# Performance work log

Measured on AMD Instinct MI355X. Metric: run time of the kernel, lower is better.

Reference implementation:

```python
import jax, jax.numpy as jnp
import numpy as np

NCE_T = 0.07   # opt.nce_T
EPS = 1e-8     # torch CosineSimilarity eps
DIAG_FILL = -10.0

N, D = 8192, 256

def setup_inputs() -> dict:
    key = jax.random.key(0)
    kq, kk = jax.random.split(key)
    feat_q = jax.random.normal(kq, (N, D), dtype=jnp.float32)
    feat_k = jax.random.normal(kk, (N, D), dtype=jnp.float32)
    return {"feat_q": feat_q, "feat_k": feat_k}

def reference(feat_q, feat_k):
    # feat_k is detached in the original
    feat_k = jax.lax.stop_gradient(feat_k)
    nq = jnp.linalg.norm(feat_q, axis=-1)            # [N]
    nk = jnp.linalg.norm(feat_k, axis=-1)            # [N]
    # positive cosine similarity (paired rows)
    l_pos = jnp.sum(feat_q * feat_k, axis=-1) / jnp.maximum(nq * nk, EPS)  # [N]
    # full N x N cosine similarity via GEMM (torch does a broadcasted version)
    sim = (feat_q @ feat_k.T) / jnp.maximum(nq[:, None] * nk[None, :], EPS)  # [N,N]
    # mask self-similarities with -10.0 BEFORE dividing by temperature
    diag = jnp.eye(sim.shape[0], dtype=bool)
    l_neg = jnp.where(diag, DIAG_FILL, sim)
    out = jnp.concatenate([l_pos[:, None], l_neg], axis=1) / NCE_T  # [N, N+1]
    # cross-entropy vs target class 0, reduction='none'
    loss = jax.scipy.special.logsumexp(out, axis=1) - out[:, 0]     # [N]
    return loss
```

## Files before the change

kernel.cpp:

```cpp
#include <hip/hip_runtime.h>
#include <stdint.h>
#include <math.h>

#define NROWS 8192
#define DDIM  256
#define BM    128
#define BN    128
#define GJ    8
#define COLS_PER_GROUP (NROWS / GJ)

constexpr float INV_T  = 1.0f / 0.07f;
constexpr float LOG2E  = 1.44269504f;
constexpr float K1     = INV_T * LOG2E;

typedef __bf16 bf16x8 __attribute__((ext_vector_type(8)));
typedef float  f32x4  __attribute__((ext_vector_type(4)));

__device__ __forceinline__ void async_copy16(const uint16_t* g, uint16_t* l) {
    __builtin_amdgcn_global_load_lds(
        (const __attribute__((address_space(1))) uint32_t*)g,
        (__attribute__((address_space(3))) uint32_t*)l, 16, 0, 0);
}

__device__ inline uint16_t f2bf(float f) {
    uint32_t u = __float_as_uint(f);
    u += 0x7fffu + ((u >> 16) & 1u);
    return (uint16_t)(u >> 16);
}

__global__ __launch_bounds__(256) void norm_convert_kernel(
    const float* __restrict__ fq, const float* __restrict__ fk,
    uint16_t* __restrict__ qb, uint16_t* __restrict__ kb)
{
    const int wave = threadIdx.x >> 6;
    const int lane = threadIdx.x & 63;
    const int row  = blockIdx.x * 4 + wave;

    const float* src; uint16_t* dstb;
    if (row < NROWS) {
        src = fq + (size_t)row * DDIM; dstb = qb + (size_t)row * DDIM;
    } else {
        int r = row - NROWS;
        src = fk + (size_t)r * DDIM; dstb = kb + (size_t)r * DDIM;
    }

    float4 v = ((const float4*)src)[lane];
    float ss = v.x*v.x + v.y*v.y + v.z*v.z + v.w*v.w;
    #pragma unroll
    for (int m = 1; m < 64; m <<= 1) ss += __shfl_xor(ss, m, 64);
    float r = rsqrtf(ss);

    ushort4 o;
    o.x = f2bf(v.x * r); o.y = f2bf(v.y * r); o.z = f2bf(v.z * r); o.w = f2bf(v.w * r);
    ((ushort4*)dstb)[lane] = o;
}

__global__ __launch_bounds__(512, 2) void nce_main_kernel(
    const uint16_t* __restrict__ qb, const uint16_t* __restrict__ kb,
    float* __restrict__ lpT, float* __restrict__ gpl)
{
    __shared__ __align__(16) uint16_t lds_k[4 * BN * 32];

    const int tid    = threadIdx.x;
    const int wave   = tid >> 6;
    const int lane   = tid & 63;
    const int quad   = lane >> 4;
    const int lanelo = lane & 15;
    const int wr     = wave >> 1;
    const int wc     = wave & 1;
    const int rowBase      = blockIdx.x * BM;
    const int colGroupBase = blockIdx.y * COLS_PER_GROUP;

    bf16x8 aq[2][8];
    #pragma unroll
    for (int mt = 0; mt < 2; ++mt) {
        const uint16_t* qrow =
            qb + (size_t)(rowBase + wr * 32 + mt * 16 + lanelo) * DDIM + quad * 8;
        #pragma unroll
        for (int kk = 0; kk < 8; ++kk)
            aq[mt][kk] = *(const bf16x8*)(qrow + kk * 32);
    }

    const int kS   = wave * 64 + lane;
    const int krow = kS >> 2;
    const int kch  = (lane & 3) ^ ((krow >> 2) & 3);
    const uint16_t* kbase = kb + (size_t)(colGroupBase + krow) * DDIM + kch * 8;

    #pragma unroll
    for (int p = 0; p < 3; ++p)
        async_copy16(kbase + (p << 5), lds_k + (p << 12) + (wave << 9));

    int bvoff[4];
    #pragma unroll
    for (int nt = 0; nt < 4; ++nt) {
        int rk = wc * 64 + nt * 16 + lanelo;
        bvoff[nt] = rk * 32 + (quad ^ (lanelo >> 2)) * 8;
    }

    float l_run[8];
    #pragma unroll
    for (int i = 0; i < 8; ++i) l_run[i] = 0.f;

    for (int jt = 0; jt < 8; ++jt) {
        const int colT = colGroupBase + jt * BN;

        f32x4 acc[2][4];
        #pragma unroll
        for (int mt = 0; mt < 2; ++mt)
            #pragma unroll
            for (int nt = 0; nt < 4; ++nt)
                acc[mt][nt] = (f32x4){0.f, 0.f, 0.f, 0.f};

        #pragma unroll
        for (int kk = 0; kk < 8; ++kk) {
            const int p = (jt << 3) + kk;

            asm volatile("s_waitcnt vmcnt(2)" ::: "memory");
            asm volatile("s_barrier" ::: "memory");

            {
                const int npm = (p + 3) & 63;
                const int off = ((npm >> 3) << 15) + ((npm & 7) << 5);
                async_copy16(kbase + off,
                             lds_k + (((p + 3) & 3) << 12) + (wave << 9));
            }

            bf16x8 bv[4];
            const int bufo = (p & 3) << 12;
            #pragma unroll
            for (int nt = 0; nt < 4; ++nt)
                bv[nt] = *(const bf16x8*)&lds_k[bufo + bvoff[nt]];

            __builtin_amdgcn_s_setprio(1);
            #pragma unroll
            for (int mt = 0; mt < 2; ++mt)
                #pragma unroll
                for (int nt = 0; nt < 4; ++nt)
                    acc[mt][nt] = __builtin_amdgcn_mfma_f32_16x16x32_bf16(
                        aq[mt][kk], bv[nt], acc[mt][nt], 0, 0, 0);
            __builtin_amdgcn_s_setprio(0);
        }

        int gcol[4];
        #pragma unroll
        for (int nt = 0; nt < 4; ++nt) gcol[nt] = colT + wc * 64 + nt * 16 + lanelo;
        #pragma unroll
        for (int mt = 0; mt < 2; ++mt) {
            #pragma unroll
            for (int rg = 0; rg < 4; ++rg) {
                int grow = rowBase + wr * 32 + mt * 16 + quad * 4 + rg;
                float s = 0.f;
                #pragma unroll
                for (int nt = 0; nt < 4; ++nt) {
                    float a = acc[mt][nt][rg];
                    float e = exp2f(fmaf(a, K1, -K1));
                    if (grow == gcol[nt]) { lpT[grow] = a * INV_T; e = 0.f; }
                    s += e;
                }
                l_run[mt * 4 + rg] += s;
            }
        }
    }

    #pragma unroll
    for (int i = 0; i < 8; ++i) {
        float v = l_run[i];
        v += __shfl_xor(v, 1, 64);
        v += __shfl_xor(v, 2, 64);
        v += __shfl_xor(v, 4, 64);
        v += __shfl_xor(v, 8, 64);
        l_run[i] = v;
    }

    __syncthreads();

    float* pl = (float*)lds_k;
    if (lanelo == 0) {
        #pragma unroll
        for (int mt = 0; mt < 2; ++mt)
            #pragma unroll
            for (int rg = 0; rg < 4; ++rg) {
                int lr = wr * 32 + mt * 16 + quad * 4 + rg;
                pl[wc * 128 + lr] = l_run[mt * 4 + rg];
            }
    }
    __syncthreads();
    if (tid < 128) {
        float L = pl[tid] + pl[128 + tid];
        gpl[(size_t)blockIdx.y * NROWS + rowBase + tid] = L;
    }
}

__global__ __launch_bounds__(256) void finalize_kernel(
    const float* __restrict__ gpl, const float* __restrict__ lpT,
    float* __restrict__ out)
{
    int t = blockIdx.x * 256 + threadIdx.x;
    if (t >= NROWS) return;
    float L = 0.f;
    #pragma unroll
    for (int g = 0; g < GJ; ++g) L += gpl[g * NROWS + t];
    float lp = lpT[t];
    L += __expf(lp - INV_T);
    out[t] = INV_T + __logf(L) - lp;
}

extern "C" void kernel_launch(void* const* d_in, const int* in_sizes, int n_in,
                              void* d_out, int out_size, void* d_ws, size_t ws_size,
                              hipStream_t stream) {
    const float* fq = (const float*)d_in[0];
    const float* fk = (const float*)d_in[1];
    char* ws = (char*)d_ws;
    uint16_t* qb  = (uint16_t*)(ws);
    uint16_t* kb  = (uint16_t*)(ws + 4194304);
    float*    lpT = (float*)(ws + 8388608);
    float*    gpl = (float*)(ws + 8421376);

    norm_convert_kernel<<<(2 * NROWS) / 4, 256, 0, stream>>>(fq, fk, qb, kb);
    dim3 grid(NROWS / BM, GJ);
    nce_main_kernel<<<grid, 512, 0, stream>>>(qb, kb, lpT, gpl);
    finalize_kernel<<<NROWS / 256, 256, 0, stream>>>(gpl, lpT, (float*)d_out);
}
```

Baseline: 121.7 us.

## Shrink row tile to 64 and stage 64-wide K chunks per barrier

Halves the row tile per block (BM 128→64) and rearranges the 8 waves as 2 rows by 4 columns, so each wave computes 32x32 instead of 32x64. K-tiles are now staged in 64-element chunks, each a 128x64 bf16 block in a 4-deep ring with an XOR swizzle. That halves the number of barriers per column tile and doubles the grid for better CU occupancy. In exchange each K row is reused by fewer Q rows, so L2/LDS traffic per MFMA rises, and LDS use grows to 64KB.

```diff
diff --git a/kernel.cpp b/kernel.cpp
--- a/kernel.cpp
+++ b/kernel.cpp
@@ -4,10 +4,13 @@
 
 #define NROWS 8192
 #define DDIM  256
-#define BM    128
+#define BM    64
 #define BN    128
 #define GJ    8
 #define COLS_PER_GROUP (NROWS / GJ)
+#define NJT   (COLS_PER_GROUP / BN)
+#define NIV   4
+#define NP    (NJT * NIV)
 
 constexpr float INV_T  = 1.0f / 0.07f;
 constexpr float LOG2E  = 1.44269504f;
@@ -59,15 +62,15 @@
     const uint16_t* __restrict__ qb, const uint16_t* __restrict__ kb,
     float* __restrict__ lpT, float* __restrict__ gpl)
 {
-    __shared__ __align__(16) uint16_t lds_k[4 * BN * 32];
+    __shared__ __align__(16) uint16_t lds_k[4 * 8192];
 
     const int tid    = threadIdx.x;
     const int wave   = tid >> 6;
     const int lane   = tid & 63;
     const int quad   = lane >> 4;
     const int lanelo = lane & 15;
-    const int wr     = wave >> 1;
-    const int wc     = wave & 1;
+    const int wr     = wave >> 2;
+    const int wc     = wave & 3;
     const int rowBase      = blockIdx.x * BM;
     const int colGroupBase = blockIdx.y * COLS_PER_GROUP;
 
@@ -80,70 +83,78 @@
         for (int kk = 0; kk < 8; ++kk)
             aq[mt][kk] = *(const bf16x8*)(qrow + kk * 32);
     }
-
-    const int kS   = wave * 64 + lane;
-    const int krow = kS >> 2;
-    const int kch  = (lane & 3) ^ ((krow >> 2) & 3);
-    const uint16_t* kbase = kb + (size_t)(colGroupBase + krow) * DDIM + kch * 8;
-
-    #pragma unroll
-    for (int p = 0; p < 3; ++p)
-        async_copy16(kbase + (p << 5), lds_k + (p << 12) + (wave << 9));
-
-    int bvoff[4];
-    #pragma unroll
-    for (int nt = 0; nt < 4; ++nt) {
-        int rk = wc * 64 + nt * 16 + lanelo;
-        bvoff[nt] = rk * 32 + (quad ^ (lanelo >> 2)) * 8;
-    }
+    asm volatile("s_waitcnt vmcnt(0)" ::: "memory");
+
+    const int r0 = wave * 8 + (lane >> 3);
+    const int c0 = (lane & 7) ^ ((lane >> 3) & 7);
+    const uint16_t* kbase0 = kb + (size_t)(colGroupBase + r0)      * DDIM + c0 * 8;
+    const uint16_t* kbase1 = kb + (size_t)(colGroupBase + r0 + 64) * DDIM + c0 * 8;
+
+    #pragma unroll
+    for (int p = 0; p < 3; ++p) {
+        uint16_t* ld = lds_k + (p << 13) + (wave << 9);
+        async_copy16(kbase0 + (p << 6), ld);
+        async_copy16(kbase1 + (p << 6), ld + 4096);
+    }
+
+    int bvoff[2][2];
+    #pragma unroll
+    for (int kk = 0; kk < 2; ++kk)
+        #pragma unroll
+        for (int nt = 0; nt < 2; ++nt) {
+            int rk = wc * 32 + nt * 16 + lanelo;
+            bvoff[kk][nt] = rk * 64 + ((kk * 4 + quad) ^ (lanelo & 7)) * 8;
+        }
 
     float l_run[8];
     #pragma unroll
     for (int i = 0; i < 8; ++i) l_run[i] = 0.f;
 
-    for (int jt = 0; jt < 8; ++jt) {
+    for (int jt = 0; jt < NJT; ++jt) {
+        f32x4 acc[2][2];
+        #pragma unroll
+        for (int mt = 0; mt < 2; ++mt)
+            #pragma unroll
+            for (int nt = 0; nt < 2; ++nt)
+                acc[mt][nt] = (f32x4){0.f, 0.f, 0.f, 0.f};
+
+        #pragma unroll
+        for (int iv = 0; iv < NIV; ++iv) {
+            const int p = jt * NIV + iv;
+
+            asm volatile("s_waitcnt vmcnt(4)" ::: "memory");
+            asm volatile("s_barrier" ::: "memory");
+
+            {
+                const int npm = (p + 3) & (NP - 1);
+                const int off = ((npm >> 2) << 15) + ((npm & 3) << 6);
+                uint16_t* ld = lds_k + (((p + 3) & 3) << 13) + (wave << 9);
+                async_copy16(kbase0 + off, ld);
+                async_copy16(kbase1 + off, ld + 4096);
+            }
+
+            const int bufo = (p & 3) << 13;
+            #pragma unroll
+            for (int kk = 0; kk < 2; ++kk) {
+                bf16x8 bv0 = *(const bf16x8*)&lds_k[bufo + bvoff[kk][0]];
+                bf16x8 bv1 = *(const bf16x8*)&lds_k[bufo + bvoff[kk][1]];
+                const int ka = iv * 2 + kk;
+                __builtin_amdgcn_s_setprio(1);
+                #pragma unroll
+                for (int mt = 0; mt < 2; ++mt) {
+                    acc[mt][0] = __builtin_amdgcn_mfma_f32_16x16x32_bf16(
+                        aq[mt][ka], bv0, acc[mt][0], 0, 0, 0);
+                    acc[mt][1] = __builtin_amdgcn_mfma_f32_16x16x32_bf16(
+                        aq[mt][ka], bv1, acc[mt][1], 0, 0, 0);
+                }
+                __builtin_amdgcn_s_setprio(0);
+            }
+        }
+
         const int colT = colGroupBase + jt * BN;
-
-        f32x4 acc[2][4];
-        #pragma unroll
-        for (int mt = 0; mt < 2; ++mt)
-            #pragma unroll
-            for (int nt = 0; nt < 4; ++nt)
-                acc[mt][nt] = (f32x4){0.f, 0.f, 0.f, 0.f};
-
-        #pragma unroll
-        for (int kk = 0; kk < 8; ++kk) {
-            const int p = (jt << 3) + kk;
-
-            asm volatile("s_waitcnt vmcnt(2)" ::: "memory");
-            asm volatile("s_barrier" ::: "memory");
-
-            {
-                const int npm = (p + 3) & 63;
-                const int off = ((npm >> 3) << 15) + ((npm & 7) << 5);
-                async_copy16(kbase + off,
-                             lds_k + (((p + 3) & 3) << 12) + (wave << 9));
-            }
-
-            bf16x8 bv[4];
-            const int bufo = (p & 3) << 12;
-            #pragma unroll
-            for (int nt = 0; nt < 4; ++nt)
-                bv[nt] = *(const bf16x8*)&lds_k[bufo + bvoff[nt]];
-
-            __builtin_amdgcn_s_setprio(1);
-            #pragma unroll
-            for (int mt = 0; mt < 2; ++mt)
-                #pragma unroll
-                for (int nt = 0; nt < 4; ++nt)
-                    acc[mt][nt] = __builtin_amdgcn_mfma_f32_16x16x32_bf16(
-                        aq[mt][kk], bv[nt], acc[mt][nt], 0, 0, 0);
-            __builtin_amdgcn_s_setprio(0);
-        }
-
-        int gcol[4];
-        #pragma unroll
-        for (int nt = 0; nt < 4; ++nt) gcol[nt] = colT + wc * 64 + nt * 16 + lanelo;
+        int gcol[2];
+        #pragma unroll
+        for (int nt = 0; nt < 2; ++nt) gcol[nt] = colT + wc * 32 + nt * 16 + lanelo;
         #pragma unroll
         for (int mt = 0; mt < 2; ++mt) {
             #pragma unroll
@@ -151,7 +162,7 @@
                 int grow = rowBase + wr * 32 + mt * 16 + quad * 4 + rg;
                 float s = 0.f;
                 #pragma unroll
-                for (int nt = 0; nt < 4; ++nt) {
+                for (int nt = 0; nt < 2; ++nt) {
                     float a = acc[mt][nt][rg];
                     float e = exp2f(fmaf(a, K1, -K1));
                     if (grow == gcol[nt]) { lpT[grow] = a * INV_T; e = 0.f; }
@@ -181,12 +192,12 @@
             #pragma unroll
             for (int rg = 0; rg < 4; ++rg) {
                 int lr = wr * 32 + mt * 16 + quad * 4 + rg;
-                pl[wc * 128 + lr] = l_run[mt * 4 + rg];
+                pl[wc * 64 + lr] = l_run[mt * 4 + rg];
             }
     }
     __syncthreads();
-    if (tid < 128) {
-        float L = pl[tid] + pl[128 + tid];
+    if (tid < 64) {
+        float L = pl[tid] + pl[64 + tid] + pl[128 + tid] + pl[192 + tid];
         gpl[(size_t)blockIdx.y * NROWS + rowBase + tid] = L;
     }
 }
```

Result: slower. 129.5 us (+6.4%).
